# Optimization experiments

Measured on AMD Instinct MI355X. Metric: run time of the kernel, lower is better.

Reference implementation:

```python
import jax, jax.numpy as jnp
import numpy as np

BATCH = 8192
FEATS = 4096
RATE = 0.1
ANNEAL = 0.5 + 0.1  # self.anneal = 0.5 + anneal


def setup_inputs() -> dict:
    key = jax.random.key(0)
    k1, k2 = jax.random.split(key)
    inputs = jax.random.normal(k1, (BATCH, FEATS), dtype=jnp.float32)
    # standard-normal draws, one per feature (replaces the serial map_fn RNG)
    noise = jax.random.normal(k2, (FEATS,), dtype=jnp.float32)
    return {"inputs": inputs, "noise": noise}


def reference(inputs, noise):
    # SegDropout (training path), agg_method='mean', noise_type='gaussian'
    F = inputs.shape[-1]
    x_agg = jnp.mean(inputs, axis=0)                      # [F] batch-wise aggregate
    x_min = jnp.min(x_agg)
    x_max = jnp.max(x_agg)
    # quantize each feature's aggregate into one of F+1 integer bins
    bins = (F * (x_agg - x_min) / (x_max - x_min)).astype(jnp.int32)  # [F], values in [0, F]
    # unique_with_counts + gather(counts, idx) == histogram lookup per feature
    counts_per_bin = jnp.bincount(bins, length=F + 1)      # [F+1]
    counts = counts_per_bin[bins].astype(inputs.dtype)     # [F] count of each feature's bin
    dr = RATE ** (1.0 / (ANNEAL * counts))                 # annealed per-bin dropout rate
    dr = jnp.where(counts == 1.0, jnp.asarray(RATE, inputs.dtype), dr)
    sigma = jnp.sqrt(dr / (1.0 - dr))                      # [F]
    # multiplicative Gaussian noise ~ N(1, sigma) per feature
    return inputs * (1.0 + sigma * noise)
```

## Files before the change

kernel.cpp:

```cpp
#include <hip/hip_runtime.h>

#define BATCH 8192
#define FEATS 4096
#define CHUNKS 256
#define ROWS_PER_CHUNK (BATCH / CHUNKS)
#define SROWS 16
#define RBLK 64
#define KSLICES 4
#define KPER (CHUNKS / KSLICES)

typedef float v4f __attribute__((ext_vector_type(4)));


__global__ __launch_bounds__(256) void colsum_part(const float* __restrict__ in,
                                                   double* __restrict__ partials,
                                                   unsigned* __restrict__ counter) {
    if (blockIdx.x == 0 && blockIdx.y == 0 && threadIdx.x == 0) *counter = 0u;
    const int colBase = blockIdx.x * 1024 + threadIdx.x * 4;
    const int row0 = blockIdx.y * ROWS_PER_CHUNK;
    const float4* p = (const float4*)in + (size_t)row0 * (FEATS / 4) + (colBase >> 2);
    double a0 = 0.0, a1 = 0.0, a2 = 0.0, a3 = 0.0;
#pragma unroll 8
    for (int r = 0; r < ROWS_PER_CHUNK; ++r) {
        float4 v = p[(size_t)r * (FEATS / 4)];
        a0 += (double)v.x; a1 += (double)v.y; a2 += (double)v.z; a3 += (double)v.w;
    }
    double* dst = partials + (size_t)blockIdx.y * FEATS + colBase;
    dst[0] = a0; dst[1] = a1; dst[2] = a2; dst[3] = a3;
}

__global__ __launch_bounds__(256) void reduce_config(const double* __restrict__ partials,
                                                     const float* __restrict__ noise,
                                                     double* __restrict__ means,
                                                     double* __restrict__ bmin,
                                                     double* __restrict__ bmax,
                                                     float* __restrict__ scale,
                                                     unsigned* __restrict__ counter) {
    const int t = threadIdx.x;
    const int cLocal = t & 63;
    const int ks = t >> 6;
    const int c = blockIdx.x * 64 + cLocal;

    double s = 0.0;
#pragma unroll 8
    for (int k = 0; k < KPER; ++k)
        s += partials[(size_t)(ks * KPER + k) * FEATS + c];

    __shared__ double sred[KSLICES][64];
    sred[ks][cLocal] = s;
    __syncthreads();

    if (ks == 0) {
        double m = ((sred[0][cLocal] + sred[1][cLocal]) + sred[2][cLocal]) + sred[3][cLocal];
        m *= (1.0 / (double)BATCH);
        means[c] = m;
        double lmin = m, lmax = m;
#pragma unroll
        for (int off = 32; off > 0; off >>= 1) {
            lmin = fmin(lmin, __shfl_down(lmin, off));
            lmax = fmax(lmax, __shfl_down(lmax, off));
        }
        if (cLocal == 0) { bmin[blockIdx.x] = lmin; bmax[blockIdx.x] = lmax; }
    }
    __threadfence();
    __syncthreads();

    __shared__ unsigned isLast;
    if (t == 0) isLast = (atomicAdd(counter, 1u) == RBLK - 1) ? 1u : 0u;
    __syncthreads();
    if (!isLast) return;
    __threadfence();

    __shared__ unsigned s_hist[FEATS + 1];
    __shared__ double s_mm[2];
    if (t == 0) {
        double a = bmin[0], b = bmax[0];
        for (int i = 1; i < RBLK; ++i) { a = fmin(a, bmin[i]); b = fmax(b, bmax[i]); }
        s_mm[0] = a; s_mm[1] = b;
    }
    for (int i = t; i < FEATS + 1; i += 256) s_hist[i] = 0;
    __syncthreads();

    const double xmin = s_mm[0];
    const double denom = s_mm[1] - xmin;

    int binr[16];
#pragma unroll
    for (int k = 0; k < 16; ++k) {
        int c2 = t + k * 256;
        double b = ((double)FEATS * (means[c2] - xmin)) / denom;
        int bi = (int)b;
        binr[k] = bi;
        atomicAdd(&s_hist[bi], 1u);
    }
    __syncthreads();

    const double K = -2.302585092994045684017991454684364208;
#pragma unroll
    for (int k = 0; k < 16; ++k) {
        int c2 = t + k * 256;
        unsigned cnt = s_hist[binr[k]];
        double dr = (cnt == 1u) ? 0.1 : exp(K / (0.6 * (double)cnt));
        double sg = sqrt(dr / (1.0 - dr));
        scale[c2] = (float)(1.0 + sg * (double)noise[c2]);
    }
}

__global__ __launch_bounds__(256) void scale_kernel(const float4* __restrict__ in,
                                                    const float4* __restrict__ scale,
                                                    float4* __restrict__ out) {
    const int col = (blockIdx.x & 3) * 256 + threadIdx.x;
    const int row0 = (blockIdx.x >> 2) * SROWS;
    const float4 s = scale[col];
    const float4* pin = in + (size_t)row0 * (FEATS / 4) + col;
    float4* pout = out + (size_t)row0 * (FEATS / 4) + col;
#pragma unroll
    for (int r = 0; r < SROWS; ++r) {
        float4 v = pin[(size_t)r * (FEATS / 4)];
        v.x *= s.x; v.y *= s.y; v.z *= s.z; v.w *= s.w;
        v4f nv = {v.x, v.y, v.z, v.w};
        __builtin_nontemporal_store(nv, (v4f*)&pout[(size_t)r * (FEATS / 4)]);
    }
}

extern "C" void kernel_launch(void* const* d_in, const int* in_sizes, int n_in,
                              void* d_out, int out_size, void* d_ws, size_t ws_size,
                              hipStream_t stream) {
    const float* in = (const float*)d_in[0];
    const float* noise = (const float*)d_in[1];
    float* out = (float*)d_out;
    double* partials = (double*)d_ws;
    double* means = partials + (size_t)CHUNKS * FEATS;
    double* bmin = means + FEATS;
    double* bmax = bmin + RBLK;
    float* scale = (float*)(bmax + RBLK);
    unsigned* counter = (unsigned*)(scale + FEATS);

    dim3 g1(4, CHUNKS);
    colsum_part<<<g1, 256, 0, stream>>>(in, partials, counter);
    reduce_config<<<RBLK, 256, 0, stream>>>(partials, noise, means, bmin, bmax, scale, counter);
    scale_kernel<<<4 * (BATCH / SROWS), 256, 0, stream>>>(
        (const float4*)in, (const float4*)scale, (float4*)out);
}
```

Before: 276.0 us.

## Fuse three kernels into one cooperative kernel with grid syncs

```diff
diff --git a/kernel.cpp b/kernel.cpp
--- a/kernel.cpp
+++ b/kernel.cpp
@@ -1,10 +1,13 @@
 #include <hip/hip_runtime.h>
+#include <hip/hip_cooperative_groups.h>
+namespace cg = cooperative_groups;
 
 #define BATCH 8192
 #define FEATS 4096
+#define NBLK 1024
 #define CHUNKS 256
-#define ROWS_PER_CHUNK (BATCH / CHUNKS)
-#define SROWS 16
+#define RPC (BATCH / CHUNKS)
+#define SR (BATCH / NBLK)
 #define RBLK 64
 #define KSLICES 4
 #define KPER (CHUNKS / KSLICES)
@@ -12,114 +15,113 @@
 typedef float v4f __attribute__((ext_vector_type(4)));
 
 
-__global__ __launch_bounds__(256) void colsum_part(const float* __restrict__ in,
-                                                   double* __restrict__ partials,
-                                                   unsigned* __restrict__ counter) {
-    if (blockIdx.x == 0 && blockIdx.y == 0 && threadIdx.x == 0) *counter = 0u;
-    const int colBase = blockIdx.x * 1024 + threadIdx.x * 4;
-    const int row0 = blockIdx.y * ROWS_PER_CHUNK;
-    const float4* p = (const float4*)in + (size_t)row0 * (FEATS / 4) + (colBase >> 2);
-    double a0 = 0.0, a1 = 0.0, a2 = 0.0, a3 = 0.0;
-#pragma unroll 8
-    for (int r = 0; r < ROWS_PER_CHUNK; ++r) {
-        float4 v = p[(size_t)r * (FEATS / 4)];
-        a0 += (double)v.x; a1 += (double)v.y; a2 += (double)v.z; a3 += (double)v.w;
-    }
-    double* dst = partials + (size_t)blockIdx.y * FEATS + colBase;
-    dst[0] = a0; dst[1] = a1; dst[2] = a2; dst[3] = a3;
-}
-
-__global__ __launch_bounds__(256) void reduce_config(const double* __restrict__ partials,
-                                                     const float* __restrict__ noise,
-                                                     double* __restrict__ means,
-                                                     double* __restrict__ bmin,
-                                                     double* __restrict__ bmax,
-                                                     float* __restrict__ scale,
-                                                     unsigned* __restrict__ counter) {
+__global__ __launch_bounds__(256) void fused_kernel(const float* __restrict__ in,
+                                                    const float* __restrict__ noise,
+                                                    float* __restrict__ out,
+                                                    double* __restrict__ partials,
+                                                    double* __restrict__ means,
+                                                    double* __restrict__ bmin,
+                                                    double* __restrict__ bmax,
+                                                    float* __restrict__ scale) {
+    cg::grid_group grid = cg::this_grid();
     const int t = threadIdx.x;
-    const int cLocal = t & 63;
-    const int ks = t >> 6;
-    const int c = blockIdx.x * 64 + cLocal;
-
-    double s = 0.0;
-#pragma unroll 8
-    for (int k = 0; k < KPER; ++k)
-        s += partials[(size_t)(ks * KPER + k) * FEATS + c];
+    const int gid = blockIdx.x;
 
     __shared__ double sred[KSLICES][64];
-    sred[ks][cLocal] = s;
-    __syncthreads();
-
-    if (ks == 0) {
-        double m = ((sred[0][cLocal] + sred[1][cLocal]) + sred[2][cLocal]) + sred[3][cLocal];
-        m *= (1.0 / (double)BATCH);
-        means[c] = m;
-        double lmin = m, lmax = m;
-#pragma unroll
-        for (int off = 32; off > 0; off >>= 1) {
-            lmin = fmin(lmin, __shfl_down(lmin, off));
-            lmax = fmax(lmax, __shfl_down(lmax, off));
-        }
-        if (cLocal == 0) { bmin[blockIdx.x] = lmin; bmax[blockIdx.x] = lmax; }
-    }
-    __threadfence();
-    __syncthreads();
-
-    __shared__ unsigned isLast;
-    if (t == 0) isLast = (atomicAdd(counter, 1u) == RBLK - 1) ? 1u : 0u;
-    __syncthreads();
-    if (!isLast) return;
-    __threadfence();
-
     __shared__ unsigned s_hist[FEATS + 1];
     __shared__ double s_mm[2];
-    if (t == 0) {
-        double a = bmin[0], b = bmax[0];
-        for (int i = 1; i < RBLK; ++i) { a = fmin(a, bmin[i]); b = fmax(b, bmax[i]); }
-        s_mm[0] = a; s_mm[1] = b;
+
+    {
+        const int cgp = gid & 3;
+        const int ch = gid >> 2;
+        const int colBase = cgp * 1024 + t * 4;
+        const int row0 = ch * RPC;
+        const float4* p = (const float4*)in + (size_t)row0 * (FEATS / 4) + (colBase >> 2);
+        double a0 = 0.0, a1 = 0.0, a2 = 0.0, a3 = 0.0;
+#pragma unroll
+        for (int r = 0; r < RPC; ++r) {
+            float4 v = p[(size_t)r * (FEATS / 4)];
+            a0 += (double)v.x; a1 += (double)v.y; a2 += (double)v.z; a3 += (double)v.w;
+        }
+        double* dst = partials + (size_t)ch * FEATS + colBase;
+        dst[0] = a0; dst[1] = a1; dst[2] = a2; dst[3] = a3;
     }
-    for (int i = t; i < FEATS + 1; i += 256) s_hist[i] = 0;
-    __syncthreads();
+    grid.sync();
 
-    const double xmin = s_mm[0];
-    const double denom = s_mm[1] - xmin;
+    if (gid < RBLK) {
+        const int cL = t & 63;
+        const int ks = t >> 6;
+        const int c = gid * 64 + cL;
+        double s = 0.0;
+#pragma unroll 8
+        for (int k = 0; k < KPER; ++k)
+            s += partials[(size_t)(ks * KPER + k) * FEATS + c];
+        sred[ks][cL] = s;
+        __syncthreads();
+        if (ks == 0) {
+            double m = ((sred[0][cL] + sred[1][cL]) + sred[2][cL]) + sred[3][cL];
+            m *= (1.0 / (double)BATCH);
+            means[c] = m;
+            double lmin = m, lmax = m;
+#pragma unroll
+            for (int off = 32; off > 0; off >>= 1) {
+                lmin = fmin(lmin, __shfl_down(lmin, off));
+                lmax = fmax(lmax, __shfl_down(lmax, off));
+            }
+            if (cL == 0) { bmin[gid] = lmin; bmax[gid] = lmax; }
+        }
+    }
+    grid.sync();
 
-    int binr[16];
+    if (gid == 0) {
+        if (t == 0) {
+            double a = bmin[0], b = bmax[0];
+            for (int i = 1; i < RBLK; ++i) { a = fmin(a, bmin[i]); b = fmax(b, bmax[i]); }
+            s_mm[0] = a; s_mm[1] = b;
+        }
+        for (int i = t; i < FEATS + 1; i += 256) s_hist[i] = 0;
+        __syncthreads();
+        const double xmin = s_mm[0];
+        const double denom = s_mm[1] - xmin;
+        int binr[16];
 #pragma unroll
-    for (int k = 0; k < 16; ++k) {
-        int c2 = t + k * 256;
-        double b = ((double)FEATS * (means[c2] - xmin)) / denom;
-        int bi = (int)b;
-        binr[k] = bi;
-        atomicAdd(&s_hist[bi], 1u);
+        for (int k = 0; k < 16; ++k) {
+            int c2 = t + k * 256;
+            double b = ((double)FEATS * (means[c2] - xmin)) / denom;
+            int bi = (int)b;
+            binr[k] = bi;
+            atomicAdd(&s_hist[bi], 1u);
+        }
+        __syncthreads();
+        const double K = -2.302585092994045684017991454684364208;
+#pragma unroll
+        for (int k = 0; k < 16; ++k) {
+            int c2 = t + k * 256;
+            unsigned cnt = s_hist[binr[k]];
+            double dr = (cnt == 1u) ? 0.1 : exp(K / (0.6 * (double)cnt));
+            double sg = sqrt(dr / (1.0 - dr));
+            scale[c2] = (float)(1.0 + sg * (double)noise[c2]);
+        }
     }
-    __syncthreads();
+    grid.sync();
 
-    const double K = -2.302585092994045684017991454684364208;
+    {
+        const float4* sc4 = (const float4*)scale;
+        const int row0 = gid * SR;
 #pragma unroll
-    for (int k = 0; k < 16; ++k) {
-        int c2 = t + k * 256;
-        unsigned cnt = s_hist[binr[k]];
-        double dr = (cnt == 1u) ? 0.1 : exp(K / (0.6 * (double)cnt));
-        double sg = sqrt(dr / (1.0 - dr));
-        scale[c2] = (float)(1.0 + sg * (double)noise[c2]);
-    }
-}
-
-__global__ __launch_bounds__(256) void scale_kernel(const float4* __restrict__ in,
-                                                    const float4* __restrict__ scale,
-                                                    float4* __restrict__ out) {
-    const int col = (blockIdx.x & 3) * 256 + threadIdx.x;
-    const int row0 = (blockIdx.x >> 2) * SROWS;
-    const float4 s = scale[col];
-    const float4* pin = in + (size_t)row0 * (FEATS / 4) + col;
-    float4* pout = out + (size_t)row0 * (FEATS / 4) + col;
+        for (int ccb = 0; ccb < 4; ++ccb) {
+            const int col = ccb * 256 + t;
+            const float4 s = sc4[col];
+            const float4* pin = (const float4*)in + (size_t)row0 * (FEATS / 4) + col;
+            float4* pout = (float4*)out + (size_t)row0 * (FEATS / 4) + col;
 #pragma unroll
-    for (int r = 0; r < SROWS; ++r) {
-        float4 v = pin[(size_t)r * (FEATS / 4)];
-        v.x *= s.x; v.y *= s.y; v.z *= s.z; v.w *= s.w;
-        v4f nv = {v.x, v.y, v.z, v.w};
-        __builtin_nontemporal_store(nv, (v4f*)&pout[(size_t)r * (FEATS / 4)]);
+            for (int r = 0; r < SR; ++r) {
+                float4 v = pin[(size_t)r * (FEATS / 4)];
+                v.x *= s.x; v.y *= s.y; v.z *= s.z; v.w *= s.w;
+                v4f nv = {v.x, v.y, v.z, v.w};
+                __builtin_nontemporal_store(nv, (v4f*)&pout[(size_t)r * (FEATS / 4)]);
+            }
+        }
     }
 }
 
@@ -134,11 +136,9 @@
     double* bmin = means + FEATS;
     double* bmax = bmin + RBLK;
     float* scale = (float*)(bmax + RBLK);
-    unsigned* counter = (unsigned*)(scale + FEATS);
 
-    dim3 g1(4, CHUNKS);
-    colsum_part<<<g1, 256, 0, stream>>>(in, partials, counter);
-    reduce_config<<<RBLK, 256, 0, stream>>>(partials, noise, means, bmin, bmax, scale, counter);
-    scale_kernel<<<4 * (BATCH / SROWS), 256, 0, stream>>>(
-        (const float4*)in, (const float4*)scale, (float4*)out);
+    void* args[] = {(void*)&in, (void*)&noise, (void*)&out, (void*)&partials,
+                    (void*)&means, (void*)&bmin, (void*)&bmax, (void*)&scale};
+    hipLaunchCooperativeKernel((const void*)fused_kernel, dim3(NBLK), dim3(256),
+                               args, 0, stream);
 }
```

After: 601.2 us. 2.18x slower.
